# Performance work log

Measured on AMD Instinct MI355X. Metric: run time of the kernel, lower is better.

The kernel has to match this reference:

```python
import jax, jax.numpy as jnp
import numpy as np


def gru_step(x, h, W, U, b):
    # Keras GRU, reset_after=True. W:[in,3H] U:[H,3H] b:[2,3H]
    gi = x @ W + b[0]
    gh = h @ U + b[1]
    iz, ir, ih = jnp.split(gi, 3, axis=-1)
    hz, hr, hh = jnp.split(gh, 3, axis=-1)
    z = jax.nn.sigmoid(iz + hz)
    r = jax.nn.sigmoid(ir + hr)
    n = jnp.tanh(ih + r * hh)
    return z * h + (1.0 - z) * n


def gru_seq(x, W, U, b):
    # x: [B,S,in] -> outputs [B,S,H], last state [B,H]; zero initial state
    B = x.shape[0]
    H = U.shape[0]
    h0 = jnp.zeros((B, H), x.dtype)
    def step(h, xt):
        h2 = gru_step(xt, h, W, U, b)
        return h2, h2
    hT, ys = jax.lax.scan(step, h0, jnp.swapaxes(x, 0, 1))
    return jnp.swapaxes(ys, 0, 1), hT


def setup_inputs() -> dict:
    key = jax.random.key(0)
    ks = jax.random.split(key, 24)
    V_en, V_fr, E, H = 32000, 32000, 256, 1024
    B, S = 32, 48
    s = 0.05
    d = {}
    d["inputs"] = jax.random.randint(ks[0], (B, S), 0, V_en, dtype=jnp.int32)
    d["gen_seq_len"] = 32
    d["start_id"] = 1
    d["emb_en"] = jax.random.normal(ks[1], (V_en, E), jnp.float32) * s
    d["emb_fr"] = jax.random.normal(ks[2], (V_fr, E), jnp.float32) * s
    # encoder GRUs: layer0 in=E, layer1 in=H
    d["enc_W0"] = jax.random.normal(ks[3], (E, 3 * H), jnp.float32) * s
    d["enc_U0"] = jax.random.normal(ks[4], (H, 3 * H), jnp.float32) * s
    d["enc_b0"] = jnp.zeros((2, 3 * H), jnp.float32)
    d["enc_W1"] = jax.random.normal(ks[5], (H, 3 * H), jnp.float32) * s
    d["enc_U1"] = jax.random.normal(ks[6], (H, 3 * H), jnp.float32) * s
    d["enc_b1"] = jnp.zeros((2, 3 * H), jnp.float32)
    # decoder GRUs: layer0 in = H(context)+E(embed), layer1 in = H
    d["dec_W0"] = jax.random.normal(ks[7], (H + E, 3 * H), jnp.float32) * s
    d["dec_U0"] = jax.random.normal(ks[8], (H, 3 * H), jnp.float32) * s
    d["dec_b0"] = jnp.zeros((2, 3 * H), jnp.float32)
    d["dec_W1"] = jax.random.normal(ks[9], (H, 3 * H), jnp.float32) * s
    d["dec_U1"] = jax.random.normal(ks[10], (H, 3 * H), jnp.float32) * s
    d["dec_b1"] = jnp.zeros((2, 3 * H), jnp.float32)
    # Bahdanau attention
    d["attn_W1"] = jax.random.normal(ks[11], (H, H), jnp.float32) * s
    d["attn_b1"] = jnp.zeros((H,), jnp.float32)
    d["attn_W2"] = jax.random.normal(ks[12], (H, H), jnp.float32) * s
    d["attn_b2"] = jnp.zeros((H,), jnp.float32)
    d["attn_V"] = jax.random.normal(ks[13], (H, 1), jnp.float32) * s
    d["attn_Vb"] = jnp.zeros((1,), jnp.float32)
    # output projection
    d["fc_W"] = jax.random.normal(ks[14], (H, V_fr), jnp.float32) * s
    d["fc_b"] = jnp.zeros((V_fr,), jnp.float32)
    return d


def reference(inputs, gen_seq_len, start_id, emb_en, emb_fr,
              enc_W0, enc_U0, enc_b0, enc_W1, enc_U1, enc_b1,
              dec_W0, dec_U0, dec_b0, dec_W1, dec_U1, dec_b1,
              attn_W1, attn_b1, attn_W2, attn_b2, attn_V, attn_Vb,
              fc_W, fc_b):
    B = inputs.shape[0]
    H = enc_U0.shape[0]
    V_fr = fc_W.shape[1]
    # ---- encoder ----
    x = emb_en[inputs]                       # [B,S,E]
    x, _ = gru_seq(x, enc_W0, enc_U0, enc_b0)
    enc_out, enc_hidden = gru_seq(x, enc_W1, enc_U1, enc_b1)  # [B,S,H], [B,H]
    # precompute W2(values) (same math as recomputing per step)
    enc_proj = enc_out @ attn_W2 + attn_b2   # [B,S,H]
    zeros_h = jnp.zeros((B, H), jnp.float32)

    def dec_step(carry, _):
        dec_in, hidden = carry
        # Bahdanau attention
        q = hidden @ attn_W1 + attn_b1                          # [B,H]
        score = jnp.tanh(q[:, None, :] + enc_proj) @ attn_V + attn_Vb  # [B,S,1]
        w = jax.nn.softmax(score, axis=1)
        ctx = jnp.sum(w * enc_out, axis=1)                      # [B,H]
        xt = jnp.concatenate([ctx, emb_fr[dec_in]], axis=-1)    # [B,H+E]
        # decoder GRUs with state reset to zero each step (initial_state=None)
        h1 = gru_step(xt, zeros_h, dec_W0, dec_U0, dec_b0)
        h2 = gru_step(h1, zeros_h, dec_W1, dec_U1, dec_b1)
        logits = h2 @ fc_W + fc_b                               # [B,V_fr]
        nxt = jnp.argmax(logits, axis=1).astype(jnp.int32)
        return (nxt, h2), logits

    dec_in0 = jnp.full((B,), start_id, dtype=jnp.int32)
    (_, _), logits_seq = jax.lax.scan(dec_step, (dec_in0, enc_hidden),
                                      None, length=gen_seq_len - 1)
    first = jax.nn.one_hot(dec_in0, V_fr, dtype=jnp.float32)[:, None, :]
    return jnp.concatenate([first, jnp.swapaxes(logits_seq, 0, 1)], axis=1)
```

## Files before the change

### kernel.cpp

```cpp
#include <hip/hip_runtime.h>
#include <math.h>

#define BB 32
#define SS 48
#define HH 1024
#define EE 256
#define VOC 32000
#define GEN 32
#define G3 3072
#define CH 256
#define NLOG (VOC / 128)

typedef float v4f __attribute__((ext_vector_type(4)));

__device__ __forceinline__ float sigf(float x) { return 1.f / (1.f + expf(-x)); }

__global__ __launch_bounds__(256) void embed_en_k(const int* __restrict__ inputs,
                                                  const float* __restrict__ emb,
                                                  float* __restrict__ x) {
    int i = blockIdx.x * 256 + threadIdx.x;
    int row = i >> 8;
    int e = i & 255;
    x[i] = emb[(size_t)inputs[row] * EE + e];
}

__global__ __launch_bounds__(256) void transpose_k(const float* __restrict__ U,
                                                   float* __restrict__ UT,
                                                   int R, int C) {
    __shared__ float t[32][33];
    int tx = threadIdx.x & 31, ty = threadIdx.x >> 5;
    int bx = blockIdx.x * 32;
    int by = blockIdx.y * 32;
#pragma unroll
    for (int i = 0; i < 4; ++i)
        t[ty + 8 * i][tx] = U[(size_t)(by + ty + 8 * i) * C + bx + tx];
    __syncthreads();
#pragma unroll
    for (int i = 0; i < 4; ++i)
        UT[(size_t)(bx + ty + 8 * i) * R + by + tx] = t[tx][ty + 8 * i];
}

__global__ __launch_bounds__(256) void gemm64(const float* __restrict__ A,
                                              const float* __restrict__ Bm,
                                              const float* __restrict__ bias,
                                              float* __restrict__ C,
                                              int N, int K) {
    __shared__ float As[32][68];
    __shared__ float Bs[32][68];
    int tid = threadIdx.x;
    int tx = tid & 15, ty = tid >> 4;
    int arow = blockIdx.y * 64, bcol = blockIdx.x * 64;
    int am = tid >> 2;
    int aq = tid & 3;
    int bk = tid >> 4;
    int bn = tid & 15;
    float acc[4][4] = {};
    for (int k0 = 0; k0 < K; k0 += 32) {
        float4 a0 = *(const float4*)(A + (size_t)(arow + am) * K + k0 + aq * 8);
        float4 a1 = *(const float4*)(A + (size_t)(arow + am) * K + k0 + aq * 8 + 4);
        float4 b0 = *(const float4*)(Bm + (size_t)(k0 + bk) * N + bcol + bn * 4);
        float4 b1 = *(const float4*)(Bm + (size_t)(k0 + bk + 16) * N + bcol + bn * 4);
        __syncthreads();
        As[aq * 8 + 0][am] = a0.x; As[aq * 8 + 1][am] = a0.y;
        As[aq * 8 + 2][am] = a0.z; As[aq * 8 + 3][am] = a0.w;
        As[aq * 8 + 4][am] = a1.x; As[aq * 8 + 5][am] = a1.y;
        As[aq * 8 + 6][am] = a1.z; As[aq * 8 + 7][am] = a1.w;
        *(float4*)&Bs[bk][bn * 4] = b0;
        *(float4*)&Bs[bk + 16][bn * 4] = b1;
        __syncthreads();
#pragma unroll
        for (int kk = 0; kk < 32; ++kk) {
            float4 a = *(const float4*)&As[kk][ty * 4];
            float4 b = *(const float4*)&Bs[kk][tx * 4];
            acc[0][0] += a.x * b.x; acc[0][1] += a.x * b.y;
            acc[0][2] += a.x * b.z; acc[0][3] += a.x * b.w;
            acc[1][0] += a.y * b.x; acc[1][1] += a.y * b.y;
            acc[1][2] += a.y * b.z; acc[1][3] += a.y * b.w;
            acc[2][0] += a.z * b.x; acc[2][1] += a.z * b.y;
            acc[2][2] += a.z * b.z; acc[2][3] += a.z * b.w;
            acc[3][0] += a.w * b.x; acc[3][1] += a.w * b.y;
            acc[3][2] += a.w * b.z; acc[3][3] += a.w * b.w;
        }
    }
    float4 bb = *(const float4*)&bias[bcol + tx * 4];
#pragma unroll
    for (int i = 0; i < 4; ++i) {
        size_t row = arow + ty * 4 + i;
        *(float4*)(C + row * N + bcol + tx * 4) =
            make_float4(acc[i][0] + bb.x, acc[i][1] + bb.y,
                        acc[i][2] + bb.z, acc[i][3] + bb.w);
    }
}

__global__ __launch_bounds__(384) void enc_step(
    const float* __restrict__ gi,
    const float* __restrict__ UT,
    const float* __restrict__ b1,
    const float* __restrict__ hin,
    float* __restrict__ hout,
    float* __restrict__ seqout,
    int t) {
    __shared__ float hs[32][260];
    __shared__ float ghs[12][33];
    const int tid = threadIdx.x;
    const int c0 = blockIdx.x * 4;
    const int ks = tid & 31;
    const int outIdx = tid >> 5;
    const int cq = outIdx >> 2;
    const int mo = outIdx & 3;
    const float* Ubase = UT + (size_t)(cq * HH + c0) * HH;
    float acc[4][8];
#pragma unroll
    for (int a = 0; a < 4; ++a)
#pragma unroll
        for (int b = 0; b < 8; ++b) acc[a][b] = 0.f;
    for (int ch = 0; ch < HH / CH; ++ch) {
        for (int i = tid; i < 32 * 64; i += 384) {
            int m = i >> 6, q = i & 63;
            *(float4*)&hs[m][q * 4] =
                *(const float4*)&hin[m * HH + ch * CH + q * 4];
        }
        __syncthreads();
#pragma unroll
        for (int j = 0; j < 2; ++j) {
            int kq = (j * 32 + ks) * 4;
            float4 uv[4];
#pragma unroll
            for (int ci = 0; ci < 4; ++ci)
                uv[ci] = *(const float4*)&Ubase[(size_t)ci * HH + ch * CH + kq];
#pragma unroll
            for (int mi = 0; mi < 8; ++mi) {
                float4 hv = *(const float4*)&hs[mo * 8 + mi][kq];
#pragma unroll
                for (int ci = 0; ci < 4; ++ci)
                    acc[ci][mi] += hv.x * uv[ci].x + hv.y * uv[ci].y +
                                   hv.z * uv[ci].z + hv.w * uv[ci].w;
            }
        }
        __syncthreads();
    }
#pragma unroll
    for (int ci = 0; ci < 4; ++ci)
#pragma unroll
        for (int mi = 0; mi < 8; ++mi) {
            float v = acc[ci][mi];
            v += __shfl_xor(v, 1, 64);
            v += __shfl_xor(v, 2, 64);
            v += __shfl_xor(v, 4, 64);
            v += __shfl_xor(v, 8, 64);
            v += __shfl_xor(v, 16, 64);
            if (ks == 0) ghs[cq * 4 + ci][mo * 8 + mi] = v;
        }
    __syncthreads();
    if (tid < 128) {
        int m = tid & 31, c = tid >> 5;
        int col = c0 + c;
        float ghz = ghs[c][m] + b1[col];
        float ghr = ghs[4 + c][m] + b1[HH + col];
        float ghh = ghs[8 + c][m] + b1[2 * HH + col];
        const float* gir = gi + ((size_t)m * SS + t) * G3;
        float z = sigf(gir[col] + ghz);
        float r = sigf(gir[HH + col] + ghr);
        float nn = tanhf(gir[2 * HH + col] + r * ghh);
        float h = z * hin[m * HH + col] + (1.f - z) * nn;
        hout[m * HH + col] = h;
        seqout[((size_t)m * SS + t) * HH + col] = h;
    }
}

__global__ __launch_bounds__(384) void dec_step(
    const float* __restrict__ xt, int K,
    const float* __restrict__ WT,
    const float* __restrict__ b0, const float* __restrict__ b1,
    float* __restrict__ hout) {
    __shared__ float hs[32][260];
    __shared__ float ghs[12][33];
    const int tid = threadIdx.x;
    const int c0 = blockIdx.x * 4;
    const int ks = tid & 31;
    const int outIdx = tid >> 5;
    const int cq = outIdx >> 2;
    const int mo = outIdx & 3;
    const float* Ubase = WT + (size_t)(cq * HH + c0) * K;
    float acc[4][8];
#pragma unroll
    for (int a = 0; a < 4; ++a)
#pragma unroll
        for (int b = 0; b < 8; ++b) acc[a][b] = 0.f;
    const int nch = K / CH;
    for (int ch = 0; ch < nch; ++ch) {
        for (int i = tid; i < 32 * 64; i += 384) {
            int m = i >> 6, q = i & 63;
            *(float4*)&hs[m][q * 4] =
                *(const float4*)&xt[(size_t)m * K + ch * CH + q * 4];
        }
        __syncthreads();
#pragma unroll
        for (int j = 0; j < 2; ++j) {
            int kq = (j * 32 + ks) * 4;
            float4 uv[4];
#pragma unroll
            for (int ci = 0; ci < 4; ++ci)
                uv[ci] = *(const float4*)&Ubase[(size_t)ci * K + ch * CH + kq];
#pragma unroll
            for (int mi = 0; mi < 8; ++mi) {
                float4 hv = *(const float4*)&hs[mo * 8 + mi][kq];
#pragma unroll
                for (int ci = 0; ci < 4; ++ci)
                    acc[ci][mi] += hv.x * uv[ci].x + hv.y * uv[ci].y +
                                   hv.z * uv[ci].z + hv.w * uv[ci].w;
            }
        }
        __syncthreads();
    }
#pragma unroll
    for (int ci = 0; ci < 4; ++ci)
#pragma unroll
        for (int mi = 0; mi < 8; ++mi) {
            float v = acc[ci][mi];
            v += __shfl_xor(v, 1, 64);
            v += __shfl_xor(v, 2, 64);
            v += __shfl_xor(v, 4, 64);
            v += __shfl_xor(v, 8, 64);
            v += __shfl_xor(v, 16, 64);
            if (ks == 0) ghs[cq * 4 + ci][mo * 8 + mi] = v;
        }
    __syncthreads();
    if (tid < 128) {
        int m = tid & 31, c = tid >> 5;
        int col = c0 + c;
        float z = sigf(ghs[c][m] + b0[col] + b1[col]);
        float r = sigf(ghs[4 + c][m] + b0[HH + col] + b1[HH + col]);
        float nn = tanhf(ghs[8 + c][m] + b0[2 * HH + col] + r * b1[2 * HH + col]);
        hout[m * HH + col] = (1.f - z) * nn;
    }
}

__global__ __launch_bounds__(256) void logits_q(const float* __restrict__ A,
                                                const float* __restrict__ fcW,
                                                const float* __restrict__ fcb,
                                                float* __restrict__ Cl,
                                                const float* __restrict__ qW,
                                                const float* __restrict__ qb,
                                                float* __restrict__ Cq,
                                                float* __restrict__ pmv,
                                                int* __restrict__ pmi,
                                                int qonly) {
    __shared__ float As[32][36];
    __shared__ float Bs[32][132];
    int tid = threadIdx.x;
    int bid = blockIdx.x;
    bool isq = qonly || (bid >= NLOG);
    const float* Bm = isq ? qW : fcW;
    const float* bias = isq ? qb : fcb;
    float* C = isq ? Cq : Cl;
    int N = isq ? HH : VOC;
    int ldc = isq ? HH : GEN * VOC;
    int bcol = (isq ? (qonly ? bid : bid - NLOG) : bid) * 128;
    int nc = tid & 15, mg = (tid >> 4) & 7, ksl = tid >> 7;
    const int nch = HH / 32;
    int am = tid >> 3, aq = tid & 7;
    float4 ra = *(const float4*)(A + (size_t)am * HH + aq * 4);
    float4 rb[4];
#pragma unroll
    for (int it = 0; it < 4; ++it) {
        int lin = it * 256 + tid;
        int k = lin >> 5, q = lin & 31;
        const float* p = Bm + (size_t)k * N + bcol + q * 4;
        if (isq) { rb[it] = *(const float4*)p; }
        else { v4f v = __builtin_nontemporal_load((const v4f*)p); rb[it] = *(float4*)&v; }
    }
    float acc[4][8] = {};
    for (int ch = 0; ch < nch; ++ch) {
        __syncthreads();
        As[aq * 4 + 0][am] = ra.x; As[aq * 4 + 1][am] = ra.y;
        As[aq * 4 + 2][am] = ra.z; As[aq * 4 + 3][am] = ra.w;
#pragma unroll
        for (int it = 0; it < 4; ++it) {
            int lin = it * 256 + tid;
            int k = lin >> 5, q = lin & 31;
            *(float4*)&Bs[k][q * 4] = rb[it];
        }
        __syncthreads();
        if (ch + 1 < nch) {
            int k0 = (ch + 1) * 32;
            ra = *(const float4*)(A + (size_t)am * HH + k0 + aq * 4);
#pragma unroll
            for (int it = 0; it < 4; ++it) {
                int lin = it * 256 + tid;
                int k = lin >> 5, q = lin & 31;
                const float* p = Bm + (size_t)(k0 + k) * N + bcol + q * 4;
                if (isq) { rb[it] = *(const float4*)p; }
                else { v4f v = __builtin_nontemporal_load((const v4f*)p); rb[it] = *(float4*)&v; }
            }
        }
#pragma unroll
        for (int kk = 0; kk < 16; ++kk) {
            int k2 = kk * 2 + ksl;
            float a[4], b[8];
            *(float4*)&a[0] = *(const float4*)&As[k2][mg * 4];
            *(float4*)&b[0] = *(const float4*)&Bs[k2][nc * 8];
            *(float4*)&b[4] = *(const float4*)&Bs[k2][nc * 8 + 4];
#pragma unroll
            for (int r = 0; r < 4; ++r)
#pragma unroll
                for (int j = 0; j < 8; ++j) acc[r][j] += a[r] * b[j];
        }
    }
    __syncthreads();
    float* red = &Bs[0][0];
    if (ksl == 1) {
        int p = tid & 127;
#pragma unroll
        for (int r = 0; r < 4; ++r)
#pragma unroll
            for (int j = 0; j < 8; ++j) red[p * 32 + r * 8 + j] = acc[r][j];
    }
    __syncthreads();
    if (ksl == 0) {
        int p = tid;
#pragma unroll
        for (int r = 0; r < 4; ++r)
#pragma unroll
            for (int j = 0; j < 8; ++j) acc[r][j] += red[p * 32 + r * 8 + j];
        float bb[8];
        *(float4*)&bb[0] = *(const float4*)&bias[bcol + nc * 8];
        *(float4*)&bb[4] = *(const float4*)&bias[bcol + nc * 8 + 4];
#pragma unroll
        for (int r = 0; r < 4; ++r) {
#pragma unroll
            for (int j = 0; j < 8; ++j) acc[r][j] += bb[j];
            int row = mg * 4 + r;
            float* cp = C + (size_t)row * ldc + bcol + nc * 8;
            if (isq) {
                *(float4*)cp = make_float4(acc[r][0], acc[r][1], acc[r][2], acc[r][3]);
                *(float4*)(cp + 4) = make_float4(acc[r][4], acc[r][5], acc[r][6], acc[r][7]);
            } else {
                v4f o0 = {acc[r][0], acc[r][1], acc[r][2], acc[r][3]};
                v4f o1 = {acc[r][4], acc[r][5], acc[r][6], acc[r][7]};
                __builtin_nontemporal_store(o0, (v4f*)cp);
                __builtin_nontemporal_store(o1, (v4f*)(cp + 4));
            }
        }
        if (!isq) {
#pragma unroll
            for (int r = 0; r < 4; ++r) {
                float best = acc[r][0]; int bidx = bcol + nc * 8;
#pragma unroll
                for (int j = 1; j < 8; ++j)
                    if (acc[r][j] > best) { best = acc[r][j]; bidx = bcol + nc * 8 + j; }
#pragma unroll
                for (int o = 1; o < 16; o <<= 1) {
                    float pv = __shfl_xor(best, o, 64);
                    int pi = __shfl_xor(bidx, o, 64);
                    if (pv > best || (pv == best && pi < bidx)) { best = pv; bidx = pi; }
                }
                if (nc == 0) {
                    int row = mg * 4 + r;
                    pmv[row * NLOG + bid] = best;
                    pmi[row * NLOG + bid] = bidx;
                }
            }
        }
    }
}

__global__ __launch_bounds__(512) void attn_ctx(const float* __restrict__ qb,
                                                const float* __restrict__ enc_proj,
                                                const float* __restrict__ enc_out,
                                                const float* __restrict__ vvec,
                                                const float* __restrict__ vb,
                                                const float* __restrict__ emb_fr,
                                                const int* __restrict__ start_id,
                                                const float* __restrict__ pmv,
                                                const int* __restrict__ pmi,
                                                int nb,
                                                float* __restrict__ xt) {
    int b = blockIdx.x;
    int tid = threadIdx.x;
    int wave = tid >> 6, lane = tid & 63;
    __shared__ float sc[SS];
    __shared__ float wsm[SS];
    __shared__ float sv[256];
    __shared__ int si[256];
    __shared__ int stok;
    if (nb == 0) {
        if (tid == 0) stok = start_id[0];
    } else {
        if (tid < 256) {
            float best = -3.4e38f; int bi = 0x7fffffff;
            for (int i = tid; i < nb; i += 256) {
                float v = pmv[(size_t)b * nb + i];
                int ix = pmi[(size_t)b * nb + i];
                if (v > best || (v == best && ix < bi)) { best = v; bi = ix; }
            }
            sv[tid] = best; si[tid] = bi;
        }
        __syncthreads();
        for (int s = 128; s; s >>= 1) {
            if (tid < s) {
                if (sv[tid + s] > sv[tid] ||
                    (sv[tid + s] == sv[tid] && si[tid + s] < si[tid])) {
                    sv[tid] = sv[tid + s]; si[tid] = si[tid + s];
                }
            }
            __syncthreads();
        }
        if (tid == 0) stok = si[0];
    }
    const float* q = qb + (size_t)b * HH;
    for (int s = wave; s < SS; s += 8) {
        const float* ep = enc_proj + (size_t)(b * SS + s) * HH;
        float sum = 0.f;
        for (int h = lane; h < HH; h += 64)
            sum += tanhf(q[h] + ep[h]) * vvec[h];
#pragma unroll
        for (int o = 32; o; o >>= 1) sum += __shfl_xor(sum, o, 64);
        if (lane == 0) sc[s] = sum + vb[0];
    }
    __syncthreads();
    if (tid < 64) {
        float v = (lane < SS) ? sc[lane] : -3.4e38f;
        float m = v;
#pragma unroll
        for (int o = 32; o; o >>= 1) m = fmaxf(m, __shfl_xor(m, o, 64));
        float e = (lane < SS) ? expf(v - m) : 0.f;
        float ssum = e;
#pragma unroll
        for (int o = 32; o; o >>= 1) ssum += __shfl_xor(ssum, o, 64);
        if (lane < SS) wsm[lane] = e / ssum;
    }
    __syncthreads();
    if (tid < 256) {
        float4 cx = make_float4(0.f, 0.f, 0.f, 0.f);
#pragma unroll 4
        for (int s = 0; s < SS; ++s) {
            float w = wsm[s];
            float4 e = *(const float4*)&enc_out[(size_t)(b * SS + s) * HH + tid * 4];
            cx.x += w * e.x; cx.y += w * e.y; cx.z += w * e.z; cx.w += w * e.w;
        }
        *(float4*)&xt[(size_t)b * (HH + EE) + tid * 4] = cx;
        xt[(size_t)b * (HH + EE) + HH + tid] = emb_fr[(size_t)stok * EE + tid];
    }
}

__global__ __launch_bounds__(256) void init_dec(float* __restrict__ out,
                                                const int* __restrict__ start_id) {
    int idx = blockIdx.x * 256 + threadIdx.x;
    int sid = start_id[0];
    int b = idx / VOC, v = idx % VOC;
    out[(size_t)b * (GEN * VOC) + v] = (v == sid) ? 1.f : 0.f;
}

extern "C" void kernel_launch(void* const* d_in, const int* in_sizes, int n_in,
                              void* d_out, int out_size, void* d_ws, size_t ws_size,
                              hipStream_t stream) {
    const int*   inputs   = (const int*)d_in[0];
    const int*   start_id = (const int*)d_in[2];
    const float* emb_en   = (const float*)d_in[3];
    const float* emb_fr   = (const float*)d_in[4];
    const float* enc_W0   = (const float*)d_in[5];
    const float* enc_U0   = (const float*)d_in[6];
    const float* enc_b0   = (const float*)d_in[7];
    const float* enc_W1   = (const float*)d_in[8];
    const float* enc_U1   = (const float*)d_in[9];
    const float* enc_b1   = (const float*)d_in[10];
    const float* dec_W0   = (const float*)d_in[11];
    const float* dec_b0   = (const float*)d_in[13];
    const float* dec_W1   = (const float*)d_in[14];
    const float* dec_b1   = (const float*)d_in[16];
    const float* attn_W1  = (const float*)d_in[17];
    const float* attn_b1  = (const float*)d_in[18];
    const float* attn_W2  = (const float*)d_in[19];
    const float* attn_b2  = (const float*)d_in[20];
    const float* attn_V   = (const float*)d_in[21];
    const float* attn_Vb  = (const float*)d_in[22];
    const float* fc_W     = (const float*)d_in[23];
    const float* fc_b     = (const float*)d_in[24];
    float* out = (float*)d_out;
    float* ws  = (float*)d_ws;

    float* giA   = ws;
    float* x_emb = giA + (size_t)BB * SS * G3;
    float* seq0  = x_emb + (size_t)BB * SS * EE;
    float* encO  = seq0 + (size_t)BB * SS * HH;
    float* encP  = encO + (size_t)BB * SS * HH;
    float* h0A   = encP + (size_t)BB * SS * HH;
    float* h0B   = h0A + BB * HH;
    float* h1A   = h0B + BB * HH;
    float* h1B   = h1A + BB * HH;
    float* qbuf  = h1B + BB * HH;
    float* xt    = qbuf + BB * HH;
    float* h1buf = xt + BB * (HH + EE);
    float* pmv   = h1buf + BB * HH;
    int*   pmi   = (int*)(pmv + 32 * NLOG);
    float* U0T   = (float*)(pmi + 32 * NLOG);
    float* U1T   = U0T + (size_t)G3 * HH;
    float* W0Td  = giA;
    float* W1Td  = U0T;

    embed_en_k<<<(BB * SS * EE) / 256, 256, 0, stream>>>(inputs, emb_en, x_emb);
    gemm64<<<dim3(G3 / 64, (BB * SS) / 64), 256, 0, stream>>>(
        x_emb, enc_W0, enc_b0, giA, G3, EE);
    transpose_k<<<dim3(96, 32), 256, 0, stream>>>(enc_U0, U0T, HH, G3);
    transpose_k<<<dim3(96, 32), 256, 0, stream>>>(enc_U1, U1T, HH, G3);
    hipMemsetAsync(h0A, 0, BB * HH * sizeof(float), stream);
    for (int t = 0; t < SS; ++t) {
        const float* hin = (t & 1) ? h0B : h0A;
        float* hout = (t & 1) ? h0A : h0B;
        enc_step<<<256, 384, 0, stream>>>(giA, U0T, enc_b0 + G3, hin, hout, seq0, t);
    }
    gemm64<<<dim3(G3 / 64, (BB * SS) / 64), 256, 0, stream>>>(
        seq0, enc_W1, enc_b1, giA, G3, HH);
    hipMemsetAsync(h1A, 0, BB * HH * sizeof(float), stream);
    for (int t = 0; t < SS; ++t) {
        const float* hin = (t & 1) ? h1B : h1A;
        float* hout = (t & 1) ? h1A : h1B;
        enc_step<<<256, 384, 0, stream>>>(giA, U1T, enc_b1 + G3, hin, hout, encO, t);
    }
    gemm64<<<dim3(HH / 64, (BB * SS) / 64), 256, 0, stream>>>(
        encO, attn_W2, attn_b2, encP, HH, HH);

    transpose_k<<<dim3(96, 40), 256, 0, stream>>>(dec_W0, W0Td, HH + EE, G3);
    transpose_k<<<dim3(96, 32), 256, 0, stream>>>(dec_W1, W1Td, HH, G3);

    init_dec<<<(BB * VOC) / 256, 256, 0, stream>>>(out, start_id);
    logits_q<<<HH / 128, 256, 0, stream>>>(h1A, fc_W, fc_b, out,
                                           attn_W1, attn_b1, qbuf, pmv, pmi, 1);
    for (int step = 1; step < GEN; ++step) {
        attn_ctx<<<BB, 512, 0, stream>>>(qbuf, encP, encO, attn_V, attn_Vb,
                                         emb_fr, start_id, pmv, pmi,
                                         (step == 1) ? 0 : NLOG, xt);
        dec_step<<<256, 384, 0, stream>>>(xt, HH + EE, W0Td, dec_b0,
                                          dec_b0 + G3, h1buf);
        dec_step<<<256, 384, 0, stream>>>(h1buf, HH, W1Td, dec_b1,
                                          dec_b1 + G3, h1A);
        logits_q<<<NLOG + HH / 128, 256, 0, stream>>>(h1A, fc_W, fc_b,
                                                      out + (size_t)step * VOC,
                                                      attn_W1, attn_b1, qbuf,
                                                      pmv, pmi, 0);
    }
}
```

Baseline: 7.155 ms.

## Fuse decoder loop into one persistent kernel with global flag barriers

Replaces the per-step decoder launches (attention, two GRU layers, logits) with a single persistent kernel of 256 blocks. The phases are separated by a software grid barrier built on per-block atomic flags, and cross-block data moves through relaxed atomic loads and stores. The attention query projection moves into the attention phase as a per-batch GEMV on a pre-transposed attn_W1, and the encoder hidden state now seeds h1A directly. This removes about 120 kernel launches and their gaps. In exchange it assumes all 256 blocks are co-resident, which risks deadlock otherwise, and the attention phase uses only 32 blocks while each one does a serial 1024x1024 GEMV.

```diff
diff --git a/kernel.cpp b/kernel.cpp
--- a/kernel.cpp
+++ b/kernel.cpp
@@ -12,6 +12,7 @@
 #define NLOG (VOC / 128)
 
 typedef float v4f __attribute__((ext_vector_type(4)));
+typedef unsigned long long ull;
 
 __device__ __forceinline__ float sigf(float x) { return 1.f / (1.f + expf(-x)); }
 
@@ -168,20 +169,27 @@
     }
 }
 
-__global__ __launch_bounds__(384) void dec_step(
-    const float* __restrict__ xt, int K,
-    const float* __restrict__ WT,
-    const float* __restrict__ b0, const float* __restrict__ b1,
-    float* __restrict__ hout) {
-    __shared__ float hs[32][260];
-    __shared__ float ghs[12][33];
-    const int tid = threadIdx.x;
-    const int c0 = blockIdx.x * 4;
+__global__ __launch_bounds__(256) void init_dec(float* __restrict__ out,
+                                                const int* __restrict__ start_id) {
+    int idx = blockIdx.x * 256 + threadIdx.x;
+    int sid = start_id[0];
+    int b = idx / VOC, v = idx % VOC;
+    out[(size_t)b * (GEN * VOC) + v] = (v == sid) ? 1.f : 0.f;
+}
+
+
+__device__ __forceinline__ void dec_phase(float* smem, const float* xt, int K,
+                                          const float* WT, const float* b0,
+                                          const float* b1, float* hout,
+                                          int tid, int c0) {
+    float (*hs)[260] = (float(*)[260])smem;
+    float (*ghs)[33] = (float(*)[33])(smem + 32 * 260);
     const int ks = tid & 31;
     const int outIdx = tid >> 5;
     const int cq = outIdx >> 2;
     const int mo = outIdx & 3;
     const float* Ubase = WT + (size_t)(cq * HH + c0) * K;
+    const ull* xt8 = (const ull*)xt;
     float acc[4][8];
 #pragma unroll
     for (int a = 0; a < 4; ++a)
@@ -189,10 +197,11 @@
         for (int b = 0; b < 8; ++b) acc[a][b] = 0.f;
     const int nch = K / CH;
     for (int ch = 0; ch < nch; ++ch) {
-        for (int i = tid; i < 32 * 64; i += 384) {
-            int m = i >> 6, q = i & 63;
-            *(float4*)&hs[m][q * 4] =
-                *(const float4*)&xt[(size_t)m * K + ch * CH + q * 4];
+        for (int i = tid; i < 32 * 128; i += 384) {
+            int m = i >> 7, q = i & 127;
+            ull v = __hip_atomic_load(&xt8[((size_t)m * K + ch * CH) / 2 + q],
+                                      __ATOMIC_RELAXED, __HIP_MEMORY_SCOPE_AGENT);
+            *(ull*)&hs[m][q * 2] = v;
         }
         __syncthreads();
 #pragma unroll
@@ -232,166 +241,35 @@
         float z = sigf(ghs[c][m] + b0[col] + b1[col]);
         float r = sigf(ghs[4 + c][m] + b0[HH + col] + b1[HH + col]);
         float nn = tanhf(ghs[8 + c][m] + b0[2 * HH + col] + r * b1[2 * HH + col]);
-        hout[m * HH + col] = (1.f - z) * nn;
-    }
-}
-
-__global__ __launch_bounds__(256) void logits_q(const float* __restrict__ A,
-                                                const float* __restrict__ fcW,
-                                                const float* __restrict__ fcb,
-                                                float* __restrict__ Cl,
-                                                const float* __restrict__ qW,
-                                                const float* __restrict__ qb,
-                                                float* __restrict__ Cq,
-                                                float* __restrict__ pmv,
-                                                int* __restrict__ pmi,
-                                                int qonly) {
-    __shared__ float As[32][36];
-    __shared__ float Bs[32][132];
-    int tid = threadIdx.x;
-    int bid = blockIdx.x;
-    bool isq = qonly || (bid >= NLOG);
-    const float* Bm = isq ? qW : fcW;
-    const float* bias = isq ? qb : fcb;
-    float* C = isq ? Cq : Cl;
-    int N = isq ? HH : VOC;
-    int ldc = isq ? HH : GEN * VOC;
-    int bcol = (isq ? (qonly ? bid : bid - NLOG) : bid) * 128;
-    int nc = tid & 15, mg = (tid >> 4) & 7, ksl = tid >> 7;
-    const int nch = HH / 32;
-    int am = tid >> 3, aq = tid & 7;
-    float4 ra = *(const float4*)(A + (size_t)am * HH + aq * 4);
-    float4 rb[4];
-#pragma unroll
-    for (int it = 0; it < 4; ++it) {
-        int lin = it * 256 + tid;
-        int k = lin >> 5, q = lin & 31;
-        const float* p = Bm + (size_t)k * N + bcol + q * 4;
-        if (isq) { rb[it] = *(const float4*)p; }
-        else { v4f v = __builtin_nontemporal_load((const v4f*)p); rb[it] = *(float4*)&v; }
-    }
-    float acc[4][8] = {};
-    for (int ch = 0; ch < nch; ++ch) {
-        __syncthreads();
-        As[aq * 4 + 0][am] = ra.x; As[aq * 4 + 1][am] = ra.y;
-        As[aq * 4 + 2][am] = ra.z; As[aq * 4 + 3][am] = ra.w;
-#pragma unroll
-        for (int it = 0; it < 4; ++it) {
-            int lin = it * 256 + tid;
-            int k = lin >> 5, q = lin & 31;
-            *(float4*)&Bs[k][q * 4] = rb[it];
-        }
-        __syncthreads();
-        if (ch + 1 < nch) {
-            int k0 = (ch + 1) * 32;
-            ra = *(const float4*)(A + (size_t)am * HH + k0 + aq * 4);
-#pragma unroll
-            for (int it = 0; it < 4; ++it) {
-                int lin = it * 256 + tid;
-                int k = lin >> 5, q = lin & 31;
-                const float* p = Bm + (size_t)(k0 + k) * N + bcol + q * 4;
-                if (isq) { rb[it] = *(const float4*)p; }
-                else { v4f v = __builtin_nontemporal_load((const v4f*)p); rb[it] = *(float4*)&v; }
-            }
-        }
-#pragma unroll
-        for (int kk = 0; kk < 16; ++kk) {
-            int k2 = kk * 2 + ksl;
-            float a[4], b[8];
-            *(float4*)&a[0] = *(const float4*)&As[k2][mg * 4];
-            *(float4*)&b[0] = *(const float4*)&Bs[k2][nc * 8];
-            *(float4*)&b[4] = *(const float4*)&Bs[k2][nc * 8 + 4];
-#pragma unroll
-            for (int r = 0; r < 4; ++r)
-#pragma unroll
-                for (int j = 0; j < 8; ++j) acc[r][j] += a[r] * b[j];
-        }
-    }
-    __syncthreads();
-    float* red = &Bs[0][0];
-    if (ksl == 1) {
-        int p = tid & 127;
-#pragma unroll
-        for (int r = 0; r < 4; ++r)
-#pragma unroll
-            for (int j = 0; j < 8; ++j) red[p * 32 + r * 8 + j] = acc[r][j];
-    }
-    __syncthreads();
-    if (ksl == 0) {
-        int p = tid;
-#pragma unroll
-        for (int r = 0; r < 4; ++r)
-#pragma unroll
-            for (int j = 0; j < 8; ++j) acc[r][j] += red[p * 32 + r * 8 + j];
-        float bb[8];
-        *(float4*)&bb[0] = *(const float4*)&bias[bcol + nc * 8];
-        *(float4*)&bb[4] = *(const float4*)&bias[bcol + nc * 8 + 4];
-#pragma unroll
-        for (int r = 0; r < 4; ++r) {
-#pragma unroll
-            for (int j = 0; j < 8; ++j) acc[r][j] += bb[j];
-            int row = mg * 4 + r;
-            float* cp = C + (size_t)row * ldc + bcol + nc * 8;
-            if (isq) {
-                *(float4*)cp = make_float4(acc[r][0], acc[r][1], acc[r][2], acc[r][3]);
-                *(float4*)(cp + 4) = make_float4(acc[r][4], acc[r][5], acc[r][6], acc[r][7]);
-            } else {
-                v4f o0 = {acc[r][0], acc[r][1], acc[r][2], acc[r][3]};
-                v4f o1 = {acc[r][4], acc[r][5], acc[r][6], acc[r][7]};
-                __builtin_nontemporal_store(o0, (v4f*)cp);
-                __builtin_nontemporal_store(o1, (v4f*)(cp + 4));
-            }
-        }
-        if (!isq) {
-#pragma unroll
-            for (int r = 0; r < 4; ++r) {
-                float best = acc[r][0]; int bidx = bcol + nc * 8;
-#pragma unroll
-                for (int j = 1; j < 8; ++j)
-                    if (acc[r][j] > best) { best = acc[r][j]; bidx = bcol + nc * 8 + j; }
-#pragma unroll
-                for (int o = 1; o < 16; o <<= 1) {
-                    float pv = __shfl_xor(best, o, 64);
-                    int pi = __shfl_xor(bidx, o, 64);
-                    if (pv > best || (pv == best && pi < bidx)) { best = pv; bidx = pi; }
-                }
-                if (nc == 0) {
-                    int row = mg * 4 + r;
-                    pmv[row * NLOG + bid] = best;
-                    pmi[row * NLOG + bid] = bidx;
-                }
-            }
-        }
-    }
-}
-
-__global__ __launch_bounds__(512) void attn_ctx(const float* __restrict__ qb,
-                                                const float* __restrict__ enc_proj,
-                                                const float* __restrict__ enc_out,
-                                                const float* __restrict__ vvec,
-                                                const float* __restrict__ vb,
-                                                const float* __restrict__ emb_fr,
-                                                const int* __restrict__ start_id,
-                                                const float* __restrict__ pmv,
-                                                const int* __restrict__ pmi,
-                                                int nb,
-                                                float* __restrict__ xt) {
-    int b = blockIdx.x;
-    int tid = threadIdx.x;
+        __hip_atomic_store(&hout[m * HH + col], (1.f - z) * nn,
+                           __ATOMIC_RELAXED, __HIP_MEMORY_SCOPE_AGENT);
+    }
+}
+
+__device__ __forceinline__ void attn_phase(
+    float* smem, int b, const float* encP_, const float* encO_,
+    const float* vvec, const float* vb, const float* emb_fr,
+    const int* start_id, const float* W1qT, const float* qb1,
+    const float* h1A, const float* pmv, const int* pmi, int nb,
+    float* xt, int tid) {
+    float* hq   = smem;
+    float* qld  = smem + 1024;
+    float* sc   = smem + 2048;
+    float* wsm  = smem + 2112;
+    float* sv   = smem + 2176;
+    int*   si   = (int*)(smem + 2432);
+    int*   stokp= (int*)(smem + 2688);
     int wave = tid >> 6, lane = tid & 63;
-    __shared__ float sc[SS];
-    __shared__ float wsm[SS];
-    __shared__ float sv[256];
-    __shared__ int si[256];
-    __shared__ int stok;
     if (nb == 0) {
-        if (tid == 0) stok = start_id[0];
+        if (tid == 0) *stokp = start_id[0];
     } else {
         if (tid < 256) {
             float best = -3.4e38f; int bi = 0x7fffffff;
             for (int i = tid; i < nb; i += 256) {
-                float v = pmv[(size_t)b * nb + i];
-                int ix = pmi[(size_t)b * nb + i];
+                float v = __hip_atomic_load((float*)&pmv[(size_t)b * nb + i],
+                                            __ATOMIC_RELAXED, __HIP_MEMORY_SCOPE_AGENT);
+                int ix = __hip_atomic_load((int*)&pmi[(size_t)b * nb + i],
+                                           __ATOMIC_RELAXED, __HIP_MEMORY_SCOPE_AGENT);
                 if (v > best || (v == best && ix < bi)) { best = v; bi = ix; }
             }
             sv[tid] = best; si[tid] = bi;
@@ -406,14 +284,28 @@
             }
             __syncthreads();
         }
-        if (tid == 0) stok = si[0];
-    }
-    const float* q = qb + (size_t)b * HH;
-    for (int s = wave; s < SS; s += 8) {
-        const float* ep = enc_proj + (size_t)(b * SS + s) * HH;
+        if (tid == 0) *stokp = si[0];
+    }
+    for (int i = tid; i < HH; i += 384)
+        hq[i] = __hip_atomic_load((float*)&h1A[(size_t)b * HH + i],
+                                  __ATOMIC_RELAXED, __HIP_MEMORY_SCOPE_AGENT);
+    __syncthreads();
+    for (int c = tid; c < HH; c += 384) {
+        const float* wr = W1qT + (size_t)c * HH;
+        float a0 = 0, a1 = 0, a2 = 0, a3 = 0;
+        for (int k = 0; k < HH; k += 4) {
+            float4 w = *(const float4*)(wr + k);
+            a0 += hq[k] * w.x;     a1 += hq[k + 1] * w.y;
+            a2 += hq[k + 2] * w.z; a3 += hq[k + 3] * w.w;
+        }
+        qld[c] = a0 + a1 + a2 + a3 + qb1[c];
+    }
+    __syncthreads();
+    for (int s = wave; s < SS; s += 6) {
+        const float* ep = encP_ + (size_t)(b * SS + s) * HH;
         float sum = 0.f;
         for (int h = lane; h < HH; h += 64)
-            sum += tanhf(q[h] + ep[h]) * vvec[h];
+            sum += tanhf(qld[h] + ep[h]) * vvec[h];
 #pragma unroll
         for (int o = 32; o; o >>= 1) sum += __shfl_xor(sum, o, 64);
         if (lane == 0) sc[s] = sum + vb[0];
@@ -436,20 +328,186 @@
 #pragma unroll 4
         for (int s = 0; s < SS; ++s) {
             float w = wsm[s];
-            float4 e = *(const float4*)&enc_out[(size_t)(b * SS + s) * HH + tid * 4];
+            float4 e = *(const float4*)&encO_[(size_t)(b * SS + s) * HH + tid * 4];
             cx.x += w * e.x; cx.y += w * e.y; cx.z += w * e.z; cx.w += w * e.w;
         }
-        *(float4*)&xt[(size_t)b * (HH + EE) + tid * 4] = cx;
-        xt[(size_t)b * (HH + EE) + HH + tid] = emb_fr[(size_t)stok * EE + tid];
-    }
-}
-
-__global__ __launch_bounds__(256) void init_dec(float* __restrict__ out,
-                                                const int* __restrict__ start_id) {
-    int idx = blockIdx.x * 256 + threadIdx.x;
-    int sid = start_id[0];
-    int b = idx / VOC, v = idx % VOC;
-    out[(size_t)b * (GEN * VOC) + v] = (v == sid) ? 1.f : 0.f;
+        size_t base = (size_t)b * (HH + EE) + tid * 4;
+        __hip_atomic_store(&xt[base + 0], cx.x, __ATOMIC_RELAXED, __HIP_MEMORY_SCOPE_AGENT);
+        __hip_atomic_store(&xt[base + 1], cx.y, __ATOMIC_RELAXED, __HIP_MEMORY_SCOPE_AGENT);
+        __hip_atomic_store(&xt[base + 2], cx.z, __ATOMIC_RELAXED, __HIP_MEMORY_SCOPE_AGENT);
+        __hip_atomic_store(&xt[base + 3], cx.w, __ATOMIC_RELAXED, __HIP_MEMORY_SCOPE_AGENT);
+        int tok = *stokp;
+        __hip_atomic_store(&xt[(size_t)b * (HH + EE) + HH + tid],
+                           emb_fr[(size_t)tok * EE + tid],
+                           __ATOMIC_RELAXED, __HIP_MEMORY_SCOPE_AGENT);
+    }
+}
+
+__device__ __forceinline__ void logits_phase(
+    float* smem, int bid, int step, const float* h1A,
+    const float* fcW, const float* fcb, float* out,
+    float* pmv, int* pmi, int tid) {
+    float (*As)[36]  = (float(*)[36])smem;
+    float (*Bs)[132] = (float(*)[132])(smem + 1152);
+    int bcol = bid * 128;
+    int nc = tid & 15, mg = (tid >> 4) & 7, ksl = (tid >> 7) & 1;
+    const int nch = HH / 32;
+    const ull* A8 = (const ull*)h1A;
+    float* Cl = out + (size_t)step * VOC;
+    const int ldc = GEN * VOC;
+    float4 rb[3];
+#pragma unroll
+    for (int it = 0; it < 3; ++it) {
+        int lin = it * 384 + tid;
+        if (lin < 1024) {
+            int k = lin >> 5, q = lin & 31;
+            v4f v = __builtin_nontemporal_load(
+                (const v4f*)(fcW + (size_t)k * VOC + bcol + q * 4));
+            rb[it] = *(float4*)&v;
+        }
+    }
+    float acc[4][8] = {};
+    for (int ch = 0; ch < nch; ++ch) {
+        __syncthreads();
+#pragma unroll
+        for (int it = 0; it < 3; ++it) {
+            int lin = it * 384 + tid;
+            if (lin < 1024) {
+                int k = lin >> 5, q = lin & 31;
+                *(float4*)&Bs[k][q * 4] = rb[it];
+            }
+        }
+        for (int lin = tid; lin < 256; lin += 384) {
+            int am = lin >> 3, aq = lin & 7;
+            size_t off = ((size_t)am * HH + ch * 32 + aq * 4) / 2;
+            ull v0 = __hip_atomic_load(&A8[off], __ATOMIC_RELAXED, __HIP_MEMORY_SCOPE_AGENT);
+            ull v1 = __hip_atomic_load(&A8[off + 1], __ATOMIC_RELAXED, __HIP_MEMORY_SCOPE_AGENT);
+            float2 f0 = *(float2*)&v0, f1 = *(float2*)&v1;
+            As[aq * 4 + 0][am] = f0.x; As[aq * 4 + 1][am] = f0.y;
+            As[aq * 4 + 2][am] = f1.x; As[aq * 4 + 3][am] = f1.y;
+        }
+        __syncthreads();
+        if (ch + 1 < nch) {
+#pragma unroll
+            for (int it = 0; it < 3; ++it) {
+                int lin = it * 384 + tid;
+                if (lin < 1024) {
+                    int k = lin >> 5, q = lin & 31;
+                    v4f v = __builtin_nontemporal_load(
+                        (const v4f*)(fcW + (size_t)((ch + 1) * 32 + k) * VOC + bcol + q * 4));
+                    rb[it] = *(float4*)&v;
+                }
+            }
+        }
+        if (tid < 256) {
+#pragma unroll
+            for (int kk = 0; kk < 16; ++kk) {
+                int k2 = kk * 2 + ksl;
+                float a[4], b[8];
+                *(float4*)&a[0] = *(const float4*)&As[k2][mg * 4];
+                *(float4*)&b[0] = *(const float4*)&Bs[k2][nc * 8];
+                *(float4*)&b[4] = *(const float4*)&Bs[k2][nc * 8 + 4];
+#pragma unroll
+                for (int r = 0; r < 4; ++r)
+#pragma unroll
+                    for (int j = 0; j < 8; ++j) acc[r][j] += a[r] * b[j];
+            }
+        }
+    }
+    __syncthreads();
+    float* red = smem + 1152;
+    if (tid < 256 && ksl == 1) {
+        int p = tid & 127;
+#pragma unroll
+        for (int r = 0; r < 4; ++r)
+#pragma unroll
+            for (int j = 0; j < 8; ++j) red[p * 32 + r * 8 + j] = acc[r][j];
+    }
+    __syncthreads();
+    if (tid < 256 && ksl == 0) {
+        int p = tid;
+#pragma unroll
+        for (int r = 0; r < 4; ++r)
+#pragma unroll
+            for (int j = 0; j < 8; ++j) acc[r][j] += red[p * 32 + r * 8 + j];
+        float bb[8];
+        *(float4*)&bb[0] = *(const float4*)&fcb[bcol + nc * 8];
+        *(float4*)&bb[4] = *(const float4*)&fcb[bcol + nc * 8 + 4];
+#pragma unroll
+        for (int r = 0; r < 4; ++r) {
+#pragma unroll
+            for (int j = 0; j < 8; ++j) acc[r][j] += bb[j];
+            int row = mg * 4 + r;
+            float* cp = Cl + (size_t)row * ldc + bcol + nc * 8;
+            v4f o0 = {acc[r][0], acc[r][1], acc[r][2], acc[r][3]};
+            v4f o1 = {acc[r][4], acc[r][5], acc[r][6], acc[r][7]};
+            __builtin_nontemporal_store(o0, (v4f*)cp);
+            __builtin_nontemporal_store(o1, (v4f*)(cp + 4));
+        }
+#pragma unroll
+        for (int r = 0; r < 4; ++r) {
+            float best = acc[r][0]; int bidx = bcol + nc * 8;
+#pragma unroll
+            for (int j = 1; j < 8; ++j)
+                if (acc[r][j] > best) { best = acc[r][j]; bidx = bcol + nc * 8 + j; }
+#pragma unroll
+            for (int o = 1; o < 16; o <<= 1) {
+                float pv = __shfl_xor(best, o, 64);
+                int pi = __shfl_xor(bidx, o, 64);
+                if (pv > best || (pv == best && pi < bidx)) { best = pv; bidx = pi; }
+            }
+            if (nc == 0) {
+                int row = mg * 4 + r;
+                __hip_atomic_store(&pmv[row * NLOG + bid], best,
+                                   __ATOMIC_RELAXED, __HIP_MEMORY_SCOPE_AGENT);
+                __hip_atomic_store(&pmi[row * NLOG + bid], bidx,
+                                   __ATOMIC_RELAXED, __HIP_MEMORY_SCOPE_AGENT);
+            }
+        }
+    }
+}
+
+__global__ __launch_bounds__(384, 1) void dec_persist(
+    const float* __restrict__ encP, const float* __restrict__ encO,
+    const float* __restrict__ vvec, const float* __restrict__ vb,
+    const float* __restrict__ emb_fr, const int* __restrict__ start_id,
+    const float* __restrict__ W1qT, const float* __restrict__ qb1,
+    const float* __restrict__ W0T, const float* __restrict__ db0,
+    const float* __restrict__ W1T, const float* __restrict__ db1,
+    const float* __restrict__ fcW, const float* __restrict__ fcb,
+    float* __restrict__ out,
+    float* __restrict__ h1A, float* __restrict__ h1buf, float* __restrict__ xt,
+    float* __restrict__ pmv, int* __restrict__ pmi, int* __restrict__ flags) {
+    __shared__ float smem[8768];
+    const int tid = threadIdx.x;
+    const int bid = blockIdx.x;
+    int pc = 0;
+#define GBAR()                                                                  \
+    do {                                                                        \
+        ++pc;                                                                   \
+        __syncthreads();                                                        \
+        if (tid == 0)                                                           \
+            __hip_atomic_store(&flags[bid * 32], pc, __ATOMIC_RELEASE,          \
+                               __HIP_MEMORY_SCOPE_AGENT);                       \
+        if (tid < 256)                                                          \
+            while (__hip_atomic_load(&flags[tid * 32], __ATOMIC_RELAXED,        \
+                                     __HIP_MEMORY_SCOPE_AGENT) < pc) {}         \
+        __syncthreads();                                                        \
+    } while (0)
+    for (int step = 1; step < GEN; ++step) {
+        if (bid < BB)
+            attn_phase(smem, bid, encP, encO, vvec, vb, emb_fr, start_id,
+                       W1qT, qb1, h1A, pmv, pmi, (step == 1) ? 0 : NLOG, xt, tid);
+        GBAR();
+        dec_phase(smem, xt, HH + EE, W0T, db0, db0 + G3, h1buf, tid, bid * 4);
+        GBAR();
+        dec_phase(smem, h1buf, HH, W1T, db1, db1 + G3, h1A, tid, bid * 4);
+        GBAR();
+        if (bid < NLOG)
+            logits_phase(smem, bid, step, h1A, fcW, fcb, out, pmv, pmi, tid);
+        GBAR();
+    }
+#undef GBAR
 }
 
 extern "C" void kernel_launch(void* const* d_in, const int* in_sizes, int n_in,
@@ -489,13 +547,14 @@
     float* h0B   = h0A + BB * HH;
     float* h1A   = h0B + BB * HH;
     float* h1B   = h1A + BB * HH;
-    float* qbuf  = h1B + BB * HH;
-    float* xt    = qbuf + BB * HH;
+    float* xt    = h1B + BB * HH;
     float* h1buf = xt + BB * (HH + EE);
     float* pmv   = h1buf + BB * HH;
     int*   pmi   = (int*)(pmv + 32 * NLOG);
-    float* U0T   = (float*)(pmi + 32 * NLOG);
+    int*   flags = pmi + 32 * NLOG;
+    float* U0T   = (float*)(flags + 256 * 32);
     float* U1T   = U0T + (size_t)G3 * HH;
+    float* W1qT  = U1T + (size_t)G3 * HH;
     float* W0Td  = giA;
     float* W1Td  = U0T;
 
@@ -523,21 +582,12 @@
 
     transpose_k<<<dim3(96, 40), 256, 0, stream>>>(dec_W0, W0Td, HH + EE, G3);
     transpose_k<<<dim3(96, 32), 256, 0, stream>>>(dec_W1, W1Td, HH, G3);
+    transpose_k<<<dim3(32, 32), 256, 0, stream>>>(attn_W1, W1qT, HH, HH);
+    hipMemsetAsync(flags, 0, 256 * 32 * sizeof(int), stream);
 
     init_dec<<<(BB * VOC) / 256, 256, 0, stream>>>(out, start_id);
-    logits_q<<<HH / 128, 256, 0, stream>>>(h1A, fc_W, fc_b, out,
-                                           attn_W1, attn_b1, qbuf, pmv, pmi, 1);
-    for (int step = 1; step < GEN; ++step) {
-        attn_ctx<<<BB, 512, 0, stream>>>(qbuf, encP, encO, attn_V, attn_Vb,
-                                         emb_fr, start_id, pmv, pmi,
-                                         (step == 1) ? 0 : NLOG, xt);
-        dec_step<<<256, 384, 0, stream>>>(xt, HH + EE, W0Td, dec_b0,
-                                          dec_b0 + G3, h1buf);
-        dec_step<<<256, 384, 0, stream>>>(h1buf, HH, W1Td, dec_b1,
-                                          dec_b1 + G3, h1A);
-        logits_q<<<NLOG + HH / 128, 256, 0, stream>>>(h1A, fc_W, fc_b,
-                                                      out + (size_t)step * VOC,
-                                                      attn_W1, attn_b1, qbuf,
-                                                      pmv, pmi, 0);
-    }
-}
+    dec_persist<<<256, 384, 0, stream>>>(
+        encP, encO, attn_V, attn_Vb, emb_fr, start_id,
+        W1qT, attn_b1, W0Td, dec_b0, W1Td, dec_b1,
+        fc_W, fc_b, out, h1A, h1buf, xt, pmv, pmi, flags);
+}
```

After: 11.84 ms. 1.65x slower.

## Retile GRU recurrent step kernels to 16 columns per block with 64 blocks

Applied to the files above, without the earlier changes.

The encoder and decoder recurrent step kernels now give each block 16 hidden columns across all three gates, with each warp handling one column for all 32 batch rows. The grid shrinks from 256 to 64 blocks. The hidden state chunk staged in shared memory is now reused across 16 columns instead of 4, which cuts redundant hidden-state loads per block. In exchange each thread holds 96 accumulators, which raises register pressure. With only 64 blocks on a many-CU GPU, less of the machine is used and weight streaming bandwidth may drop.

```diff
diff --git a/kernel.cpp b/kernel.cpp
--- a/kernel.cpp
+++ b/kernel.cpp
@@ -92,7 +92,7 @@
     }
 }
 
-__global__ __launch_bounds__(384) void enc_step(
+__global__ __launch_bounds__(512) void enc_step64(
     const float* __restrict__ gi,
     const float* __restrict__ UT,
     const float* __restrict__ b1,
@@ -101,21 +101,21 @@
     float* __restrict__ seqout,
     int t) {
     __shared__ float hs[32][260];
-    __shared__ float ghs[12][33];
+    __shared__ float ghs[3][16][33];
     const int tid = threadIdx.x;
-    const int c0 = blockIdx.x * 4;
+    const int c0 = blockIdx.x * 16;
     const int ks = tid & 31;
-    const int outIdx = tid >> 5;
-    const int cq = outIdx >> 2;
-    const int mo = outIdx & 3;
-    const float* Ubase = UT + (size_t)(cq * HH + c0) * HH;
-    float acc[4][8];
-#pragma unroll
-    for (int a = 0; a < 4; ++a)
-#pragma unroll
-        for (int b = 0; b < 8; ++b) acc[a][b] = 0.f;
+    const int g = tid >> 5;
+    const float* U0 = UT + (size_t)(0 * HH + c0 + g) * HH;
+    const float* U1 = UT + (size_t)(1 * HH + c0 + g) * HH;
+    const float* U2 = UT + (size_t)(2 * HH + c0 + g) * HH;
+    float acc[3][32];
+#pragma unroll
+    for (int a = 0; a < 3; ++a)
+#pragma unroll
+        for (int b = 0; b < 32; ++b) acc[a][b] = 0.f;
     for (int ch = 0; ch < HH / CH; ++ch) {
-        for (int i = tid; i < 32 * 64; i += 384) {
+        for (int i = tid; i < 32 * 64; i += 512) {
             int m = i >> 6, q = i & 63;
             *(float4*)&hs[m][q * 4] =
                 *(const float4*)&hin[m * HH + ch * CH + q * 4];
@@ -124,40 +124,45 @@
 #pragma unroll
         for (int j = 0; j < 2; ++j) {
             int kq = (j * 32 + ks) * 4;
-            float4 uv[4];
-#pragma unroll
-            for (int ci = 0; ci < 4; ++ci)
-                uv[ci] = *(const float4*)&Ubase[(size_t)ci * HH + ch * CH + kq];
-#pragma unroll
-            for (int mi = 0; mi < 8; ++mi) {
-                float4 hv = *(const float4*)&hs[mo * 8 + mi][kq];
-#pragma unroll
-                for (int ci = 0; ci < 4; ++ci)
-                    acc[ci][mi] += hv.x * uv[ci].x + hv.y * uv[ci].y +
-                                   hv.z * uv[ci].z + hv.w * uv[ci].w;
-            }
-        }
-        __syncthreads();
-    }
-#pragma unroll
-    for (int ci = 0; ci < 4; ++ci)
-#pragma unroll
-        for (int mi = 0; mi < 8; ++mi) {
-            float v = acc[ci][mi];
+            float4 u0 = *(const float4*)&U0[ch * CH + kq];
+            float4 u1 = *(const float4*)&U1[ch * CH + kq];
+            float4 u2 = *(const float4*)&U2[ch * CH + kq];
+#pragma unroll
+            for (int mi = 0; mi < 32; ++mi) {
+                float4 hv = *(const float4*)&hs[mi][kq];
+                acc[0][mi] += hv.x * u0.x + hv.y * u0.y + hv.z * u0.z + hv.w * u0.w;
+                acc[1][mi] += hv.x * u1.x + hv.y * u1.y + hv.z * u1.z + hv.w * u1.w;
+                acc[2][mi] += hv.x * u2.x + hv.y * u2.y + hv.z * u2.z + hv.w * u2.w;
+            }
+        }
+        __syncthreads();
+    }
+#pragma unroll
+    for (int gate = 0; gate < 3; ++gate)
+#pragma unroll
+        for (int mi = 0; mi < 32; ++mi) {
+            float v = acc[gate][mi];
             v += __shfl_xor(v, 1, 64);
             v += __shfl_xor(v, 2, 64);
             v += __shfl_xor(v, 4, 64);
             v += __shfl_xor(v, 8, 64);
             v += __shfl_xor(v, 16, 64);
-            if (ks == 0) ghs[cq * 4 + ci][mo * 8 + mi] = v;
-        }
-    __syncthreads();
-    if (tid < 128) {
-        int m = tid & 31, c = tid >> 5;
-        int col = c0 + c;
-        float ghz = ghs[c][m] + b1[col];
-        float ghr = ghs[4 + c][m] + b1[HH + col];
-        float ghh = ghs[8 + c][m] + b1[2 * HH + col];
+            acc[gate][mi] = v;
+        }
+    if (ks == 0) {
+#pragma unroll
+        for (int gate = 0; gate < 3; ++gate)
+#pragma unroll
+            for (int mi = 0; mi < 32; ++mi)
+                ghs[gate][g][mi] = acc[gate][mi];
+    }
+    __syncthreads();
+    {
+        int col16 = tid >> 5, m = tid & 31;
+        int col = c0 + col16;
+        float ghz = ghs[0][col16][m] + b1[col];
+        float ghr = ghs[1][col16][m] + b1[HH + col];
+        float ghh = ghs[2][col16][m] + b1[2 * HH + col];
         const float* gir = gi + ((size_t)m * SS + t) * G3;
         float z = sigf(gir[col] + ghz);
         float r = sigf(gir[HH + col] + ghr);
@@ -168,28 +173,28 @@
     }
 }
 
-__global__ __launch_bounds__(384) void dec_step(
+__global__ __launch_bounds__(512) void dec_step64(
     const float* __restrict__ xt, int K,
     const float* __restrict__ WT,
     const float* __restrict__ b0, const float* __restrict__ b1,
     float* __restrict__ hout) {
     __shared__ float hs[32][260];
-    __shared__ float ghs[12][33];
+    __shared__ float ghs[3][16][33];
     const int tid = threadIdx.x;
-    const int c0 = blockIdx.x * 4;
+    const int c0 = blockIdx.x * 16;
     const int ks = tid & 31;
-    const int outIdx = tid >> 5;
-    const int cq = outIdx >> 2;
-    const int mo = outIdx & 3;
-    const float* Ubase = WT + (size_t)(cq * HH + c0) * K;
-    float acc[4][8];
-#pragma unroll
-    for (int a = 0; a < 4; ++a)
-#pragma unroll
-        for (int b = 0; b < 8; ++b) acc[a][b] = 0.f;
+    const int g = tid >> 5;
+    const float* U0 = WT + (size_t)(0 * HH + c0 + g) * K;
+    const float* U1 = WT + (size_t)(1 * HH + c0 + g) * K;
+    const float* U2 = WT + (size_t)(2 * HH + c0 + g) * K;
+    float acc[3][32];
+#pragma unroll
+    for (int a = 0; a < 3; ++a)
+#pragma unroll
+        for (int b = 0; b < 32; ++b) acc[a][b] = 0.f;
     const int nch = K / CH;
     for (int ch = 0; ch < nch; ++ch) {
-        for (int i = tid; i < 32 * 64; i += 384) {
+        for (int i = tid; i < 32 * 64; i += 512) {
             int m = i >> 6, q = i & 63;
             *(float4*)&hs[m][q * 4] =
                 *(const float4*)&xt[(size_t)m * K + ch * CH + q * 4];
@@ -198,40 +203,45 @@
 #pragma unroll
         for (int j = 0; j < 2; ++j) {
             int kq = (j * 32 + ks) * 4;
-            float4 uv[4];
-#pragma unroll
-            for (int ci = 0; ci < 4; ++ci)
-                uv[ci] = *(const float4*)&Ubase[(size_t)ci * K + ch * CH + kq];
-#pragma unroll
-            for (int mi = 0; mi < 8; ++mi) {
-                float4 hv = *(const float4*)&hs[mo * 8 + mi][kq];
-#pragma unroll
-                for (int ci = 0; ci < 4; ++ci)
-                    acc[ci][mi] += hv.x * uv[ci].x + hv.y * uv[ci].y +
-                                   hv.z * uv[ci].z + hv.w * uv[ci].w;
-            }
-        }
-        __syncthreads();
-    }
-#pragma unroll
-    for (int ci = 0; ci < 4; ++ci)
-#pragma unroll
-        for (int mi = 0; mi < 8; ++mi) {
-            float v = acc[ci][mi];
+            float4 u0 = *(const float4*)&U0[ch * CH + kq];
+            float4 u1 = *(const float4*)&U1[ch * CH + kq];
+            float4 u2 = *(const float4*)&U2[ch * CH + kq];
+#pragma unroll
+            for (int mi = 0; mi < 32; ++mi) {
+                float4 hv = *(const float4*)&hs[mi][kq];
+                acc[0][mi] += hv.x * u0.x + hv.y * u0.y + hv.z * u0.z + hv.w * u0.w;
+                acc[1][mi] += hv.x * u1.x + hv.y * u1.y + hv.z * u1.z + hv.w * u1.w;
+                acc[2][mi] += hv.x * u2.x + hv.y * u2.y + hv.z * u2.z + hv.w * u2.w;
+            }
+        }
+        __syncthreads();
+    }
+#pragma unroll
+    for (int gate = 0; gate < 3; ++gate)
+#pragma unroll
+        for (int mi = 0; mi < 32; ++mi) {
+            float v = acc[gate][mi];
             v += __shfl_xor(v, 1, 64);
             v += __shfl_xor(v, 2, 64);
             v += __shfl_xor(v, 4, 64);
             v += __shfl_xor(v, 8, 64);
             v += __shfl_xor(v, 16, 64);
-            if (ks == 0) ghs[cq * 4 + ci][mo * 8 + mi] = v;
-        }
-    __syncthreads();
-    if (tid < 128) {
-        int m = tid & 31, c = tid >> 5;
-        int col = c0 + c;
-        float z = sigf(ghs[c][m] + b0[col] + b1[col]);
-        float r = sigf(ghs[4 + c][m] + b0[HH + col] + b1[HH + col]);
-        float nn = tanhf(ghs[8 + c][m] + b0[2 * HH + col] + r * b1[2 * HH + col]);
+            acc[gate][mi] = v;
+        }
+    if (ks == 0) {
+#pragma unroll
+        for (int gate = 0; gate < 3; ++gate)
+#pragma unroll
+            for (int mi = 0; mi < 32; ++mi)
+                ghs[gate][g][mi] = acc[gate][mi];
+    }
+    __syncthreads();
+    {
+        int col16 = tid >> 5, m = tid & 31;
+        int col = c0 + col16;
+        float z = sigf(ghs[0][col16][m] + b0[col] + b1[col]);
+        float r = sigf(ghs[1][col16][m] + b0[HH + col] + b1[HH + col]);
+        float nn = tanhf(ghs[2][col16][m] + b0[2 * HH + col] + r * b1[2 * HH + col]);
         hout[m * HH + col] = (1.f - z) * nn;
     }
 }
@@ -508,7 +518,7 @@
     for (int t = 0; t < SS; ++t) {
         const float* hin = (t & 1) ? h0B : h0A;
         float* hout = (t & 1) ? h0A : h0B;
-        enc_step<<<256, 384, 0, stream>>>(giA, U0T, enc_b0 + G3, hin, hout, seq0, t);
+        enc_step64<<<64, 512, 0, stream>>>(giA, U0T, enc_b0 + G3, hin, hout, seq0, t);
     }
     gemm64<<<dim3(G3 / 64, (BB * SS) / 64), 256, 0, stream>>>(
         seq0, enc_W1, enc_b1, giA, G3, HH);
@@ -516,7 +526,7 @@
     for (int t = 0; t < SS; ++t) {
         const float* hin = (t & 1) ? h1B : h1A;
         float* hout = (t & 1) ? h1A : h1B;
-        enc_step<<<256, 384, 0, stream>>>(giA, U1T, enc_b1 + G3, hin, hout, encO, t);
+        enc_step64<<<64, 512, 0, stream>>>(giA, U1T, enc_b1 + G3, hin, hout, encO, t);
     }
     gemm64<<<dim3(HH / 64, (BB * SS) / 64), 256, 0, stream>>>(
         encO, attn_W2, attn_b2, encP, HH, HH);
@@ -531,10 +541,10 @@
         attn_ctx<<<BB, 512, 0, stream>>>(qbuf, encP, encO, attn_V, attn_Vb,
                                          emb_fr, start_id, pmv, pmi,
                                          (step == 1) ? 0 : NLOG, xt);
-        dec_step<<<256, 384, 0, stream>>>(xt, HH + EE, W0Td, dec_b0,
-                                          dec_b0 + G3, h1buf);
-        dec_step<<<256, 384, 0, stream>>>(h1buf, HH, W1Td, dec_b1,
-                                          dec_b1 + G3, h1A);
+        dec_step64<<<64, 512, 0, stream>>>(xt, HH + EE, W0Td, dec_b0,
+                                           dec_b0 + G3, h1buf);
+        dec_step64<<<64, 512, 0, stream>>>(h1buf, HH, W1Td, dec_b1,
+                                           dec_b1 + G3, h1A);
         logits_q<<<NLOG + HH / 128, 256, 0, stream>>>(h1A, fc_W, fc_b,
                                                       out + (size_t)step * VOC,
                                                       attn_W1, attn_b1, qbuf,
```

Measured after the change: 9.310 ms. 1.3x slower.
